# Kernel optimization log

Hardware: AMD Instinct MI355X
Metric: run time of the kernel (lower is better)

## Reference

```python
import jax, jax.numpy as jnp
import numpy as np

B, S, D, DK = 8192, 3, 2048, 1024  # S fixed to 3 by Linear(3,3)/Bilinear(3,3,3)
NORM_FACT = 1.0 / np.sqrt(DK)


def setup_inputs() -> dict:
    key = jax.random.key(0)
    ks = jax.random.split(key, 9)
    s_lin = 1.0 / np.sqrt(D)
    s3 = 1.0 / np.sqrt(3.0)
    return {
        "img": jax.random.normal(ks[0], (B, S, D), jnp.float32),
        "text": jax.random.normal(ks[1], (B, S, D), jnp.float32),
        "Wq": jax.random.uniform(ks[2], (DK, D), jnp.float32, -s_lin, s_lin),
        "bq": jax.random.uniform(ks[3], (DK,), jnp.float32, -s_lin, s_lin),
        "Wk": jax.random.uniform(ks[4], (DK, D), jnp.float32, -s_lin, s_lin),
        "bk": jax.random.uniform(ks[5], (DK,), jnp.float32, -s_lin, s_lin),
        "Wj": jax.random.uniform(ks[6], (3, 3), jnp.float32, -s3, s3),
        "bj": jax.random.uniform(ks[7], (3,), jnp.float32, -s3, s3),
        "Wbil": jax.random.uniform(ks[8], (3, 3, 3), jnp.float32, -s3, s3),
    }


def reference(img, text, Wq, bq, Wk, bk, Wj, bj, Wbil):
    # Projections: [B, S, DK]
    Q_i = jnp.einsum("bsd,kd->bsk", img, Wq) + bq
    K_i = jnp.einsum("bsd,kd->bsk", img, Wk) + bk
    Q_t = jnp.einsum("bsd,kd->bsk", text, Wq) + bq
    K_t = jnp.einsum("bsd,kd->bsk", text, Wk) + bk

    # [B, S, S] attention maps; note: scale applied AFTER softmax (faithful to source)
    atten_it = jax.nn.softmax(jnp.einsum("bqk,bsk->bqs", Q_i, K_t), axis=-1) * NORM_FACT
    atten_ii = jax.nn.softmax(jnp.einsum("bqk,bsk->bqs", Q_i, K_i), axis=-1) * NORM_FACT
    atten_tt = jax.nn.softmax(jnp.einsum("bqk,bsk->bqs", Q_t, K_t), axis=-1) * NORM_FACT

    def j_lin(x):  # Linear(3,3) on last dim
        return jnp.einsum("bqs,os->bqo", x, Wj) + bj

    def bilinear(x1, x2):  # Bilinear(3,3,3, bias=False)
        return jnp.einsum("bqi,oij,bqj->bqo", x1, Wbil, x2)

    j_it = j_lin(atten_it)
    atten_i = bilinear(j_it, j_lin(atten_ii))
    atten_t = bilinear(j_it, j_lin(atten_tt))

    output_i = jnp.einsum("bqs,bsd->bqd", atten_i, img)
    output_t = jnp.einsum("bqs,bsd->bqd", atten_t, text)
    return (output_i, output_t)
```

## Files before the change

### kernel.cpp

```cpp
#include <hip/hip_runtime.h>

typedef unsigned short u16;
typedef unsigned int u32;
typedef __attribute__((ext_vector_type(8))) short short8;
typedef __attribute__((ext_vector_type(4))) float f32x4;

#define GLOBAL_AS __attribute__((address_space(1)))
#define LDS_AS __attribute__((address_space(3)))

__device__ __forceinline__ u16 f2bf(float f) {
  u32 u = __float_as_uint(f);
  u += 0x7fffu + ((u >> 16) & 1u);
  return (u16)(u >> 16);
}
__device__ __forceinline__ float bflo(u32 u) { return __uint_as_float(u << 16); }
__device__ __forceinline__ float bfhi(u32 u) { return __uint_as_float(u & 0xffff0000u); }

__device__ __forceinline__ void gload_lds16(const void* g, void* l) {
  __builtin_amdgcn_global_load_lds((const GLOBAL_AS void*)g, (LDS_AS void*)l, 16, 0, 0);
}

__global__ __launch_bounds__(256) void convert_all(
    const float4* __restrict__ img4, const float4* __restrict__ text4,
    const float4* __restrict__ wq4, const float4* __restrict__ wk4,
    const float4* __restrict__ bq4, const float4* __restrict__ bk4,
    ushort4* __restrict__ xbf4, ushort4* __restrict__ wcat4,
    float4* __restrict__ bcat4) {
  size_t id = (size_t)blockIdx.x * 256 + threadIdx.x;
  if (id < 25165824) {
    float4 v = (id < 12582912) ? img4[id] : text4[id - 12582912];
    ushort4 r; r.x = f2bf(v.x); r.y = f2bf(v.y); r.z = f2bf(v.z); r.w = f2bf(v.w);
    xbf4[id] = r;
  } else if (id < 26214400) {
    size_t j = id - 25165824;
    float4 v = (j < 524288) ? wq4[j] : wk4[j - 524288];
    ushort4 r; r.x = f2bf(v.x); r.y = f2bf(v.y); r.z = f2bf(v.z); r.w = f2bf(v.w);
    wcat4[j] = r;
  } else {
    size_t j = id - 26214400;
    bcat4[j] = (j < 256) ? bq4[j] : bk4[j - 256];
  }
}

__global__ __launch_bounds__(512, 2) void gemm_qk(
    const u16* __restrict__ X, const u16* __restrict__ W,
    const float* __restrict__ bias, u16* __restrict__ QK) {
  __shared__ __align__(16) u16 Al[2][16384];
  __shared__ __align__(16) u16 Bl[2][16384];

  const int t = threadIdx.x;
  const int lane = t & 63;
  const int wv = t >> 6;
  const int wm = wv >> 2;
  const int wn = wv & 3;
  const int fm = lane & 15;
  const int fq = lane >> 4;
  const int l3 = lane >> 3;
  const int l7 = lane & 7;

  const int swz = (blockIdx.x & 7) * 192 + (blockIdx.x >> 3);
  const int m0 = (swz >> 3) * 256;
  const int n0 = (swz & 7) * 256;

  const int kswz = (l7 ^ l3) * 8;
  const int rA0 = wv * 8 + l3;
  const int rB0 = (wv >> 2) * 64 + (wv & 3) * 8 + l3;
  const u16* baseA = X + (size_t)(m0 + rA0) * 2048 + kswz;
  const u16* baseB = W + (size_t)(n0 + rB0) * 2048 + kswz;

  const int cx = fm & 7;
  const int aRd = (wm * 128 + fm) * 64;
  const int bRd = (wn * 64 + fm) * 64;

  const f32x4 zero = {0.f, 0.f, 0.f, 0.f};
  f32x4 acc[8][4];
#pragma unroll
  for (int i = 0; i < 8; i++)
#pragma unroll
    for (int j = 0; j < 4; j++) acc[i][j] = zero;

  short8 a[4][2], bl[2][2], bh[2][2];

#define STAGE_A(buf, half, tt) do {                                        \
    const u16* s_ = baseA + (size_t)(tt) * 64 + (half) * 131072;           \
    u16* d_ = &Al[buf][wv * 512 + (half) * 4096];                          \
    gload_lds16(s_, d_);                                                   \
    gload_lds16(s_ + 262144, d_ + 8192);                                   \
  } while (0)
#define STAGE_B(buf, half, tt) do {                                        \
    const u16* s_ = baseB + (size_t)(tt) * 64 + (half) * 65536;            \
    u16* d_ = &Bl[buf][(wv >> 2) * 4096 + (wv & 3) * 512 + (half) * 2048]; \
    gload_lds16(s_, d_);                                                   \
    gload_lds16(s_ + 262144, d_ + 8192);                                   \
  } while (0)

#define RD_A(buf, h) do {                                                  \
    _Pragma("unroll") for (int mi = 0; mi < 4; mi++)                       \
    _Pragma("unroll") for (int kk = 0; kk < 2; kk++)                       \
      a[mi][kk] = *(const short8*)&Al[buf][aRd + (h) * 4096 + mi * 1024 +  \
                                           ((((kk << 2) | fq) ^ cx) * 8)]; \
  } while (0)
#define RD_B(buf, h, bb) do {                                              \
    _Pragma("unroll") for (int nj = 0; nj < 2; nj++)                       \
    _Pragma("unroll") for (int kk = 0; kk < 2; kk++)                       \
      bb[nj][kk] = *(const short8*)&Bl[buf][bRd + (h) * 2048 + nj * 1024 + \
                                            ((((kk << 2) | fq) ^ cx) * 8)];\
  } while (0)

#define MM(R, Cb, bb) do {                                                 \
    __builtin_amdgcn_s_setprio(1);                                         \
    _Pragma("unroll") for (int mi = 0; mi < 4; mi++)                       \
    _Pragma("unroll") for (int nj = 0; nj < 2; nj++)                       \
    _Pragma("unroll") for (int kk = 0; kk < 2; kk++)                       \
      acc[(R) + mi][(Cb) + nj] = __builtin_amdgcn_mfma_f32_16x16x32_bf16(  \
          a[mi][kk], bb[nj][kk], acc[(R) + mi][(Cb) + nj], 0, 0, 0);       \
    __builtin_amdgcn_s_setprio(0);                                         \
  } while (0)

#define BAR1_LGKM() do {                                                   \
    asm volatile("" ::: "memory");                                         \
    __builtin_amdgcn_s_barrier();                                          \
    asm volatile("s_waitcnt lgkmcnt(0)" ::: "memory");                     \
    __builtin_amdgcn_sched_barrier(0);                                     \
  } while (0)
#define BAR2(N) do {                                                       \
    asm volatile("s_waitcnt vmcnt(" #N ")" ::: "memory");                  \
    __builtin_amdgcn_s_barrier();                                          \
    asm volatile("" ::: "memory");                                         \
  } while (0)

  STAGE_A(0, 0, 0);
  STAGE_B(0, 0, 0);
  STAGE_B(0, 1, 0);
  STAGE_A(0, 1, 0);
  asm volatile("s_waitcnt vmcnt(4)" ::: "memory");
  __builtin_amdgcn_s_barrier();
  asm volatile("" ::: "memory");

  for (int kt = 0; kt < 31; ++kt) {
    const int c = kt & 1, o = c ^ 1;
    RD_A(c, 0);
    RD_B(c, 0, bl);
    STAGE_A(o, 0, kt + 1);
    BAR1_LGKM();
    MM(0, 0, bl);
    BAR2(4);
    RD_B(c, 1, bh);
    STAGE_B(o, 0, kt + 1);
    BAR1_LGKM();
    MM(0, 2, bh);
    BAR2(4);
    RD_A(c, 1);
    STAGE_B(o, 1, kt + 1);
    BAR1_LGKM();
    MM(4, 0, bl);
    BAR2(4);
    STAGE_A(o, 1, kt + 1);
    BAR1_LGKM();
    MM(4, 2, bh);
    BAR2(4);
  }

  {
    RD_A(1, 0);
    RD_B(1, 0, bl);
    BAR1_LGKM();
    MM(0, 0, bl);
    BAR2(2);
    RD_B(1, 1, bh);
    BAR1_LGKM();
    MM(0, 2, bh);
    BAR2(0);
    RD_A(1, 1);
    BAR1_LGKM();
    MM(4, 0, bl);
    MM(4, 2, bh);
  }

  float bn[4];
#pragma unroll
  for (int j = 0; j < 4; j++) bn[j] = bias[n0 + wn * 64 + j * 16 + fm];

#pragma unroll
  for (int mi = 0; mi < 8; mi++) {
#pragma unroll
    for (int r = 0; r < 4; r++) {
      int mg = m0 + wm * 128 + mi * 16 + fq * 4 + r;
      unsigned bb, idx, base;
      if (mg < 24576) { bb = (unsigned)mg / 3u; idx = (unsigned)mg - bb * 3u; base = 0u; }
      else { unsigned mt = (unsigned)mg - 24576u; bb = mt / 3u; idx = mt - bb * 3u; base = 6u; }
      size_t rowbase = (size_t)bb * 12288 + (size_t)(base + idx) * 1024;
#pragma unroll
      for (int j = 0; j < 4; j++) {
        int ng = n0 + wn * 64 + j * 16 + fm;
        size_t pos = rowbase + ((ng & 1024) ? 3072 : 0) + (ng & 1023);
        QK[pos] = f2bf(acc[mi][j][r] + bn[j]);
      }
    }
  }
#undef STAGE_A
#undef STAGE_B
#undef RD_A
#undef RD_B
#undef MM
#undef BAR1_LGKM
#undef BAR2
}

__global__ __launch_bounds__(256) void fuse_out(
    const float* __restrict__ img, const float* __restrict__ text,
    const float* __restrict__ Wj, const float* __restrict__ bjp,
    const float* __restrict__ Wb, float* __restrict__ out) {
  const int t = threadIdx.x;
  const int lane = t & 63;
  const int wv = t >> 6;
  const int b = blockIdx.x;

  const uint2* qkp = (const uint2*)((const char*)out + (size_t)b * 24576);

  float R[12][4];
#pragma unroll
  for (int r = 0; r < 12; r++) {
    uint2 u = qkp[r * 256 + t];
    R[r][0] = bflo(u.x); R[r][1] = bfhi(u.x);
    R[r][2] = bflo(u.y); R[r][3] = bfhi(u.y);
  }
  float acc[27];
#pragma unroll
  for (int a = 0; a < 27; a++) acc[a] = 0.f;
#pragma unroll
  for (int q = 0; q < 3; q++)
#pragma unroll
    for (int s = 0; s < 3; s++)
#pragma unroll
      for (int j = 0; j < 4; j++) {
        acc[q * 3 + s]      += R[q][j]     * R[9 + s][j];
        acc[9 + q * 3 + s]  += R[q][j]     * R[3 + s][j];
        acc[18 + q * 3 + s] += R[6 + q][j] * R[9 + s][j];
      }
#pragma unroll
  for (int a = 0; a < 27; a++) {
    float v = acc[a];
#pragma unroll
    for (int off = 32; off > 0; off >>= 1) v += __shfl_xor(v, off, 64);
    acc[a] = v;
  }
  __shared__ float red[4][27];
  if (lane == 0) {
#pragma unroll
    for (int a = 0; a < 27; a++) red[wv][a] = acc[a];
  }
  __syncthreads();
  float S[27];
#pragma unroll
  for (int a = 0; a < 27; a++) S[a] = red[0][a] + red[1][a] + red[2][a] + red[3][a];

  float P[27];
#pragma unroll
  for (int m = 0; m < 3; m++)
#pragma unroll
    for (int q = 0; q < 3; q++) {
      int o0 = m * 9 + q * 3;
      float x = S[o0], y = S[o0 + 1], z = S[o0 + 2];
      float mx = fmaxf(x, fmaxf(y, z));
      float e0 = __expf(x - mx), e1 = __expf(y - mx), e2 = __expf(z - mx);
      float inv = 0.03125f / (e0 + e1 + e2);
      P[o0] = e0 * inv; P[o0 + 1] = e1 * inv; P[o0 + 2] = e2 * inv;
    }
  float J[3][3][3];
#pragma unroll
  for (int m = 0; m < 3; m++)
#pragma unroll
    for (int q = 0; q < 3; q++)
#pragma unroll
      for (int o = 0; o < 3; o++)
        J[m][q][o] = bjp[o] + Wj[o * 3 + 0] * P[m * 9 + q * 3 + 0]
                            + Wj[o * 3 + 1] * P[m * 9 + q * 3 + 1]
                            + Wj[o * 3 + 2] * P[m * 9 + q * 3 + 2];
  float ai[3][3], at[3][3];
#pragma unroll
  for (int q = 0; q < 3; q++)
#pragma unroll
    for (int o = 0; o < 3; o++) {
      float s1 = 0.f, s2 = 0.f;
#pragma unroll
      for (int i = 0; i < 3; i++) {
        float a1 = J[0][q][i];
#pragma unroll
        for (int j = 0; j < 3; j++) {
          float w = Wb[(o * 3 + i) * 3 + j];
          s1 += a1 * w * J[1][q][j];
          s2 += a1 * w * J[2][q][j];
        }
      }
      ai[q][o] = s1; at[q][o] = s2;
    }

  const float4* im4 = (const float4*)(img + (size_t)b * 6144);
  const float4* tx4 = (const float4*)(text + (size_t)b * 6144);
  float4* oi4 = (float4*)out + (size_t)b * 1536;
  float4* ot4 = (float4*)out + 12582912 + (size_t)b * 1536;
#pragma unroll
  for (int rep = 0; rep < 2; rep++) {
    int col = rep * 256 + t;
    float4 x0 = im4[col], x1 = im4[512 + col], x2 = im4[1024 + col];
    float4 y0 = tx4[col], y1 = tx4[512 + col], y2 = tx4[1024 + col];
#pragma unroll
    for (int q = 0; q < 3; q++) {
      float4 o1, o2;
      o1.x = ai[q][0] * x0.x + ai[q][1] * x1.x + ai[q][2] * x2.x;
      o1.y = ai[q][0] * x0.y + ai[q][1] * x1.y + ai[q][2] * x2.y;
      o1.z = ai[q][0] * x0.z + ai[q][1] * x1.z + ai[q][2] * x2.z;
      o1.w = ai[q][0] * x0.w + ai[q][1] * x1.w + ai[q][2] * x2.w;
      oi4[q * 512 + col] = o1;
      o2.x = at[q][0] * y0.x + at[q][1] * y1.x + at[q][2] * y2.x;
      o2.y = at[q][0] * y0.y + at[q][1] * y1.y + at[q][2] * y2.y;
      o2.z = at[q][0] * y0.z + at[q][1] * y1.z + at[q][2] * y2.z;
      o2.w = at[q][0] * y0.w + at[q][1] * y1.w + at[q][2] * y2.w;
      ot4[q * 512 + col] = o2;
    }
  }
}

extern "C" void kernel_launch(void* const* d_in, const int* in_sizes, int n_in,
                              void* d_out, int out_size, void* d_ws, size_t ws_size,
                              hipStream_t stream) {
  const float* img  = (const float*)d_in[0];
  const float* text = (const float*)d_in[1];
  const float* Wq   = (const float*)d_in[2];
  const float* bq   = (const float*)d_in[3];
  const float* Wk   = (const float*)d_in[4];
  const float* bk   = (const float*)d_in[5];
  const float* Wj   = (const float*)d_in[6];
  const float* bj   = (const float*)d_in[7];
  const float* Wbil = (const float*)d_in[8];
  float* out = (float*)d_out;

  u16* Wcat = (u16*)d_ws;
  float* bcat = (float*)((char*)d_ws + 8388608);
  u16* Xbf = (u16*)(out + 50331648);
  u16* QK  = (u16*)out;

  convert_all<<<102402, 256, 0, stream>>>(
      (const float4*)img, (const float4*)text, (const float4*)Wq,
      (const float4*)Wk, (const float4*)bq, (const float4*)bk,
      (ushort4*)Xbf, (ushort4*)Wcat, (float4*)bcat);

  gemm_qk<<<1536, 512, 0, stream>>>(Xbf, Wcat, bcat, QK);

  fuse_out<<<8192, 256, 0, stream>>>(img, text, Wj, bj, Wbil, out);
}
```

Baseline: 1.224 ms.

## Relax GEMM barrier/waitcnt schedule and map one batch per wave in fuse_out

The GEMM main loop now splits the combined barrier+waitcnt macros into finer-grained waits. It drops several vmcnt waits between phases and flattens the epilogue to fewer barriers, aiming to cut synchronization stalls. The fuse_out kernel now assigns one batch element per wavefront instead of per block, removing the LDS cross-wave reduction and __syncthreads. The relaxed waits risk reading LDS before the asynchronous global-to-LDS loads have completed.

```diff
diff --git a/kernel.cpp b/kernel.cpp
--- a/kernel.cpp
+++ b/kernel.cpp
@@ -117,65 +117,59 @@
     __builtin_amdgcn_s_setprio(0);                                         \
   } while (0)
 
-#define BAR1_LGKM() do {                                                   \
-    asm volatile("" ::: "memory");                                         \
-    __builtin_amdgcn_s_barrier();                                          \
-    asm volatile("s_waitcnt lgkmcnt(0)" ::: "memory");                     \
-    __builtin_amdgcn_sched_barrier(0);                                     \
-  } while (0)
-#define BAR2(N) do {                                                       \
-    asm volatile("s_waitcnt vmcnt(" #N ")" ::: "memory");                  \
-    __builtin_amdgcn_s_barrier();                                          \
-    asm volatile("" ::: "memory");                                         \
-  } while (0)
+#define WAIT_LGKM0() asm volatile("s_waitcnt lgkmcnt(0)" ::: "memory")
+#define BARRIER() __builtin_amdgcn_s_barrier()
 
   STAGE_A(0, 0, 0);
   STAGE_B(0, 0, 0);
   STAGE_B(0, 1, 0);
   STAGE_A(0, 1, 0);
   asm volatile("s_waitcnt vmcnt(4)" ::: "memory");
-  __builtin_amdgcn_s_barrier();
-  asm volatile("" ::: "memory");
+  BARRIER();
 
   for (int kt = 0; kt < 31; ++kt) {
     const int c = kt & 1, o = c ^ 1;
     RD_A(c, 0);
     RD_B(c, 0, bl);
     STAGE_A(o, 0, kt + 1);
-    BAR1_LGKM();
+    asm volatile("s_waitcnt lgkmcnt(8)" ::: "memory");
+    BARRIER();
+    WAIT_LGKM0();
     MM(0, 0, bl);
-    BAR2(4);
+    asm volatile("s_waitcnt vmcnt(2)" ::: "memory");
+    BARRIER();
     RD_B(c, 1, bh);
     STAGE_B(o, 0, kt + 1);
-    BAR1_LGKM();
+    BARRIER();
+    WAIT_LGKM0();
     MM(0, 2, bh);
-    BAR2(4);
+    BARRIER();
     RD_A(c, 1);
     STAGE_B(o, 1, kt + 1);
-    BAR1_LGKM();
+    BARRIER();
+    WAIT_LGKM0();
     MM(4, 0, bl);
-    BAR2(4);
+    BARRIER();
     STAGE_A(o, 1, kt + 1);
-    BAR1_LGKM();
+    BARRIER();
+    WAIT_LGKM0();
     MM(4, 2, bh);
-    BAR2(4);
-  }
-
-  {
-    RD_A(1, 0);
-    RD_B(1, 0, bl);
-    BAR1_LGKM();
-    MM(0, 0, bl);
-    BAR2(2);
-    RD_B(1, 1, bh);
-    BAR1_LGKM();
-    MM(0, 2, bh);
-    BAR2(0);
-    RD_A(1, 1);
-    BAR1_LGKM();
-    MM(4, 0, bl);
-    MM(4, 2, bh);
-  }
+    asm volatile("s_waitcnt vmcnt(4)" ::: "memory");
+    BARRIER();
+  }
+
+  asm volatile("s_waitcnt vmcnt(0)" ::: "memory");
+  BARRIER();
+  RD_A(1, 0);
+  RD_B(1, 0, bl);
+  RD_B(1, 1, bh);
+  WAIT_LGKM0();
+  MM(0, 0, bl);
+  MM(0, 2, bh);
+  RD_A(1, 1);
+  WAIT_LGKM0();
+  MM(4, 0, bl);
+  MM(4, 2, bh);
 
   float bn[4];
 #pragma unroll
@@ -203,8 +197,8 @@
 #undef RD_A
 #undef RD_B
 #undef MM
-#undef BAR1_LGKM
-#undef BAR2
+#undef WAIT_LGKM0
+#undef BARRIER
 }
 
 __global__ __launch_bounds__(256) void fuse_out(
@@ -214,30 +208,34 @@
   const int t = threadIdx.x;
   const int lane = t & 63;
   const int wv = t >> 6;
-  const int b = blockIdx.x;
+  const int b = blockIdx.x * 4 + wv;
 
   const uint2* qkp = (const uint2*)((const char*)out + (size_t)b * 24576);
 
-  float R[12][4];
-#pragma unroll
-  for (int r = 0; r < 12; r++) {
-    uint2 u = qkp[r * 256 + t];
-    R[r][0] = bflo(u.x); R[r][1] = bfhi(u.x);
-    R[r][2] = bflo(u.y); R[r][3] = bfhi(u.y);
-  }
   float acc[27];
 #pragma unroll
   for (int a = 0; a < 27; a++) acc[a] = 0.f;
-#pragma unroll
-  for (int q = 0; q < 3; q++)
-#pragma unroll
-    for (int s = 0; s < 3; s++)
-#pragma unroll
-      for (int j = 0; j < 4; j++) {
-        acc[q * 3 + s]      += R[q][j]     * R[9 + s][j];
-        acc[9 + q * 3 + s]  += R[q][j]     * R[3 + s][j];
-        acc[18 + q * 3 + s] += R[6 + q][j] * R[9 + s][j];
-      }
+
+#pragma unroll
+  for (int c = 0; c < 4; c++) {
+    float R[12][4];
+#pragma unroll
+    for (int r = 0; r < 12; r++) {
+      uint2 u = qkp[r * 256 + c * 64 + lane];
+      R[r][0] = bflo(u.x); R[r][1] = bfhi(u.x);
+      R[r][2] = bflo(u.y); R[r][3] = bfhi(u.y);
+    }
+#pragma unroll
+    for (int q = 0; q < 3; q++)
+#pragma unroll
+      for (int s = 0; s < 3; s++)
+#pragma unroll
+        for (int j = 0; j < 4; j++) {
+          acc[q * 3 + s]      += R[q][j]     * R[9 + s][j];
+          acc[9 + q * 3 + s]  += R[q][j]     * R[3 + s][j];
+          acc[18 + q * 3 + s] += R[6 + q][j] * R[9 + s][j];
+        }
+  }
 #pragma unroll
   for (int a = 0; a < 27; a++) {
     float v = acc[a];
@@ -245,15 +243,6 @@
     for (int off = 32; off > 0; off >>= 1) v += __shfl_xor(v, off, 64);
     acc[a] = v;
   }
-  __shared__ float red[4][27];
-  if (lane == 0) {
-#pragma unroll
-    for (int a = 0; a < 27; a++) red[wv][a] = acc[a];
-  }
-  __syncthreads();
-  float S[27];
-#pragma unroll
-  for (int a = 0; a < 27; a++) S[a] = red[0][a] + red[1][a] + red[2][a] + red[3][a];
 
   float P[27];
 #pragma unroll
@@ -261,7 +250,7 @@
 #pragma unroll
     for (int q = 0; q < 3; q++) {
       int o0 = m * 9 + q * 3;
-      float x = S[o0], y = S[o0 + 1], z = S[o0 + 2];
+      float x = acc[o0], y = acc[o0 + 1], z = acc[o0 + 2];
       float mx = fmaxf(x, fmaxf(y, z));
       float e0 = __expf(x - mx), e1 = __expf(y - mx), e2 = __expf(z - mx);
       float inv = 0.03125f / (e0 + e1 + e2);
@@ -301,8 +290,8 @@
   float4* oi4 = (float4*)out + (size_t)b * 1536;
   float4* ot4 = (float4*)out + 12582912 + (size_t)b * 1536;
 #pragma unroll
-  for (int rep = 0; rep < 2; rep++) {
-    int col = rep * 256 + t;
+  for (int rep = 0; rep < 8; rep++) {
+    int col = rep * 64 + lane;
     float4 x0 = im4[col], x1 = im4[512 + col], x2 = im4[1024 + col];
     float4 y0 = tx4[col], y1 = tx4[512 + col], y2 = tx4[1024 + col];
 #pragma unroll
@@ -348,5 +337,5 @@
 
   gemm_qk<<<1536, 512, 0, stream>>>(Xbf, Wcat, bcat, QK);
 
-  fuse_out<<<8192, 256, 0, stream>>>(img, text, Wj, bj, Wbil, out);
-}
+  fuse_out<<<2048, 256, 0, stream>>>(img, text, Wj, bj, Wbil, out);
+}
```

Result: no change. 1.230 ms (+0.5%).
